# Kernel tuning notes

Measured on AMD Instinct MI355X. Metric: run time of the kernel, lower is better.

## Reference

```python
import jax, jax.numpy as jnp
import numpy as np

B = 100000  # number of index rows
R1, N1, N2, N3, R2 = 1, 200, 200, 50, 32


def setup_inputs() -> dict:
    key = jax.random.key(0)
    k0, k1, k2, k3, k4 = jax.random.split(key, 5)
    TT_core = jax.random.normal(k0, (R1, N1, N2, N3, R2), dtype=jnp.float32)
    # Kernel (gram) matrices per mode, as produced by e.g. an RBF kernel on
    # side information; positive entries in [0,1) like an RBF gram matrix.
    K1 = jax.random.uniform(k1, (N1, N1), dtype=jnp.float32)
    K2 = jax.random.uniform(k2, (N2, N2), dtype=jnp.float32)
    K3 = jax.random.uniform(k3, (N3, N3), dtype=jnp.float32)
    # Multi-index: one column per tensor mode; kept in [0, 50) so it is
    # in-range for every mode (N3 = 50 is the smallest).
    indices = jax.random.randint(k4, (B, 3), 0, N3, dtype=jnp.int64)
    return {"TT_core": TT_core, "K1": K1, "K2": K2, "K3": K3, "indices": indices}


def reference(TT_core, K1, K2, K3, indices):
    # lazy_mode_product(T, K, mode) == contract K over the given tensor mode.
    # TT_core axes: (r1, i, j, k, r2)
    T = jnp.einsum('ai,rijks->rajks', K1, TT_core)   # mode 1
    T = jnp.einsum('bj,rajks->rabks', K2, T)         # mode 2
    T = jnp.einsum('ck,rabks->rabcs', K3, T)         # mode 3
    # Auxiliary regularization term (full_grad=False branch of TT_kernel_component)
    reg = T * TT_core
    # T.permute([1,2,3,0,-1])[i1,i2,i3] -> (B, r1, r2) multi-index gather
    Tp = jnp.transpose(T, (1, 2, 3, 0, 4))           # (n1, n2, n3, r1, r2)
    out = Tp[indices[:, 0], indices[:, 1], indices[:, 2]]  # (B, r1, r2)
    return out, reg
```

## Files before the change

### kernel.cpp

```cpp
#include <hip/hip_runtime.h>
#include <type_traits>


typedef float    f32x4 __attribute__((ext_vector_type(4)));
typedef float    f32x8 __attribute__((ext_vector_type(8)));
typedef _Float16 half8 __attribute__((ext_vector_type(8)));
typedef unsigned short ushort8 __attribute__((ext_vector_type(8)));
typedef unsigned short u16;
typedef unsigned int   u32;

#define N12   200
#define N3    50
#define R2    32
#define SJK   320000
#define SKS   1600
#define NTOT  64000000
#define OUT_ELEMS 3200000
#define APAD  208
#define KPAD  224
#define K3B_HALVES 4096

__global__ __launch_bounds__(256) void k_prep(
    const float* __restrict__ K1, const float* __restrict__ K2,
    const float* __restrict__ K3, u16* __restrict__ kh) {
  int t = blockIdx.x * 256 + threadIdx.x;
  const int total = APAD * KPAD;
  if (t >= 2 * total + K3B_HALVES) return;
  float x;
  if (t < 2 * total) {
    const float* src = (t < total) ? K1 : K2;
    int tt = (t < total) ? t : t - total;
    int r = tt / KPAD, c = tt % KPAD;
    x = (r < N12 && c < N12) ? src[r * N12 + c] : 0.f;
  } else {
    int u = t - 2 * total;
    int e = u & 7, l = (u >> 3) & 63, frag = u >> 9;
    int c = (frag & 3) * 16 + (l & 15);
    int k = (frag >> 2) * 32 + (l >> 4) * 8 + e;
    x = (c < N3 && k < N3) ? K3[c * N3 + k] : 0.f;
  }
  kh[t] = __builtin_bit_cast(u16, (_Float16)x);
}

#define ALOAD(S)                                                              \
  { ar0 = *(const int4*)(Ah + ((wave*4+0)*16 + arow) * KPAD + (S)*32 + acolh); \
    ar1 = *(const int4*)(Ah + ((wave*4+1)*16 + arow) * KPAD + (S)*32 + acolh); \
    ar2 = *(const int4*)(Ah + ((wave*4+2)*16 + arow) * KPAD + (S)*32 + acolh); \
    ar3 = *(const int4*)(Ah + ((wave*4+3)*16 + arow) * KPAD + (S)*32 + acolh); }

#define ASTORE(BUF)                                                           \
  { *(int4*)(&As[BUF][(wave*4+0)*512 + lane*8]) = ar0;                        \
    *(int4*)(&As[BUF][(wave*4+1)*512 + lane*8]) = ar1;                        \
    *(int4*)(&As[BUF][(wave*4+2)*512 + lane*8]) = ar2;                        \
    *(int4*)(&As[BUF][(wave*4+3)*512 + lane*8]) = ar3; }

#define LOADB(S, BV)                                                          \
  { _Pragma("unroll")                                                         \
    for (int e = 0; e < 8; ++e) {                                             \
      int kr = (S)*32 + kq + e; if (kr > 199) kr = 199;                       \
      BV[e] = bp[(long)kr * ldB]; } }

#define STAGE(S, BV)                                                          \
  { half8 bh;                                                                 \
    _Pragma("unroll")                                                         \
    for (int e = 0; e < 8; ++e) {                                             \
      if constexpr (BF32) bh[e] = (_Float16)BV[e];                            \
      else bh[e] = __builtin_bit_cast(_Float16, (u16)BV[e]);                  \
    }                                                                         \
    const u16* as_ = &As[(S)&1][0];                                           \
    _Pragma("unroll")                                                         \
    for (int t = 0; t < 13; ++t) {                                            \
      half8 ah = *(const half8*)(as_ + (t*16 + l15)*32 + kq);                 \
      acc[t] = __builtin_amdgcn_mfma_f32_16x16x32_f16(ah, bh, acc[t], 0,0,0); \
    } }

template <typename BT, typename DT>
__global__ __launch_bounds__(256, 3) void k_mfma_contract(
    const BT* __restrict__ Bsrc, const u16* __restrict__ Ah,
    DT* __restrict__ Dout, int ldB, int ldD, long bStrideB, long bStrideD) {
  constexpr bool BF32 = std::is_same_v<BT, float>;
  __shared__ __align__(16) u16 As[2][8192];
  const int lane = threadIdx.x & 63;
  const int wave = threadIdx.x >> 6;
  const int l15  = lane & 15;
  const int kg   = lane >> 4;
  const int kq   = kg * 8;
  const int arow = lane >> 2;
  const int acolh = (lane & 3) * 8;
  const int n0   = blockIdx.x * 64 + wave * 16 + l15;
  const long bb  = (long)blockIdx.y * bStrideB;
  const long db  = (long)blockIdx.y * bStrideD;
  const BT* bp = Bsrc + bb + n0;

  f32x4 acc[13];
#pragma unroll
  for (int t = 0; t < 13; ++t)
#pragma unroll
    for (int q = 0; q < 4; ++q) acc[t][q] = 0.f;

  int4 ar0, ar1, ar2, ar3;
  using BReg = std::conditional_t<BF32, f32x8, ushort8>;
  BReg B0, B1, B2, B3, B4, B5, B6;

  ALOAD(0)
  LOADB(0, B0) LOADB(1, B1) LOADB(2, B2) LOADB(3, B3)
  LOADB(4, B4) LOADB(5, B5) LOADB(6, B6)
  ASTORE(0)
  __syncthreads();

  ALOAD(1)  STAGE(0, B0)  ASTORE(1)  __syncthreads();
  ALOAD(2)  STAGE(1, B1)  ASTORE(0)  __syncthreads();
  ALOAD(3)  STAGE(2, B2)  ASTORE(1)  __syncthreads();
  ALOAD(4)  STAGE(3, B3)  ASTORE(0)  __syncthreads();
  ALOAD(5)  STAGE(4, B4)  ASTORE(1)  __syncthreads();
  ALOAD(6)  STAGE(5, B5)  ASTORE(0)  __syncthreads();
  STAGE(6, B6)

#pragma unroll
  for (int t = 0; t < 13; ++t) {
    const int rb = t * 16 + kg * 4;
#pragma unroll
    for (int r = 0; r < 4; ++r) {
      const int row = rb + r;
      if (row < N12) {
        if constexpr (std::is_same_v<DT, float>)
          Dout[db + (long)row * ldD + n0] = acc[t][r];
        else
          Dout[db + (long)row * ldD + n0] =
              __builtin_bit_cast(u16, (_Float16)acc[t][r]);
      }
    }
  }
}

__global__ __launch_bounds__(256, 8) void k_contract_k_mfma(
    const u16* __restrict__ T2h, const float* __restrict__ TT,
    const u16* __restrict__ K3B, float* __restrict__ reg) {
  __shared__ __align__(16) u16 bs[K3B_HALVES];
  const int tid  = threadIdx.x;
  {
    const int4* src = (const int4*)K3B;
    int4* dst = (int4*)bs;
    dst[tid] = src[tid];
    dst[tid + 256] = src[tid + 256];
  }
  const int lane = tid & 63;
  const int wave = tid >> 6;
  const int l15  = lane & 15;
  const int kg   = lane >> 4;
  const int ab   = blockIdx.x * 4 + wave;
  const int base = ab * SKS;
  __syncthreads();

  half8 bf[2][4];
#pragma unroll
  for (int ks = 0; ks < 2; ++ks)
#pragma unroll
    for (int cs = 0; cs < 4; ++cs)
      bf[ks][cs] = *(const half8*)(bs + ((ks * 4 + cs) * 64 + lane) * 8);

  half8 af[2][2];
#pragma unroll
  for (int rt = 0; rt < 2; ++rt)
#pragma unroll
    for (int ks = 0; ks < 2; ++ks)
#pragma unroll
      for (int e = 0; e < 8; ++e) {
        int k = ks * 32 + kg * 8 + e; if (k > 49) k = 49;
        af[rt][ks][e] =
            __builtin_bit_cast(_Float16, T2h[base + k * R2 + rt * 16 + l15]);
      }

  f32x4 acc[2][4];
#pragma unroll
  for (int rt = 0; rt < 2; ++rt)
#pragma unroll
    for (int cs = 0; cs < 4; ++cs)
#pragma unroll
      for (int q = 0; q < 4; ++q) acc[rt][cs][q] = 0.f;

#pragma unroll
  for (int rt = 0; rt < 2; ++rt)
#pragma unroll
    for (int ks = 0; ks < 2; ++ks)
#pragma unroll
      for (int cs = 0; cs < 4; ++cs)
        acc[rt][cs] = __builtin_amdgcn_mfma_f32_16x16x32_f16(
            af[rt][ks], bf[ks][cs], acc[rt][cs], 0, 0, 0);

#pragma unroll
  for (int cs = 0; cs < 4; ++cs) {
    const int c = cs * 16 + l15;
    if (c < N3) {
      const int o0 = base + c * R2 + kg * 4;
      f32x4 tv0 = *(const f32x4*)(TT + o0);
      f32x4 tv1 = *(const f32x4*)(TT + o0 + 16);
      f32x4 r0, r1;
#pragma unroll
      for (int q = 0; q < 4; ++q) {
        r0[q] = acc[0][cs][q] * tv0[q];
        r1[q] = acc[1][cs][q] * tv1[q];
      }
      *(f32x4*)(reg + o0) = r0;
      *(f32x4*)(reg + o0 + 16) = r1;
    }
  }
}

template <typename T>
__global__ __launch_bounds__(256) void k_gather(
    const T* T2, const float* __restrict__ K3,
    const int* __restrict__ idx, float* __restrict__ out) {
  int g = blockIdx.x * 256 + threadIdx.x;
  int n = g >> 5, s = g & 31;
  int a = idx[n * 3 + 0], b = idx[n * 3 + 1], c = idx[n * 3 + 2];
  const T* t2 = T2 + a * SJK + b * SKS + s;
  const float* k3r = K3 + c * N3;
  float acc = 0.f;
#pragma unroll
  for (int k = 0; k < N3; ++k) {
    float v;
    if constexpr (std::is_same_v<T, float>) v = t2[k * R2];
    else v = (float)__builtin_bit_cast(_Float16, t2[k * R2]);
    acc = fmaf(k3r[k], v, acc);
  }
  out[g] = acc;
}

__global__ __launch_bounds__(256) void k_transpose(
    const float* __restrict__ K2, float* __restrict__ K2T) {
  int t = blockIdx.x * 256 + threadIdx.x;
  if (t < N12 * N12) {
    int i = t / N12, a = t % N12;
    K2T[t] = K2[a * N12 + i];
  }
}

__global__ __launch_bounds__(256) void k_contract_j_inplace(
    float* T12, const float* __restrict__ K2T) {
  __shared__ float lds[N12 * 80];
  const int a    = blockIdx.y;
  const int m0   = blockIdx.x * 80;
  const int base = a * SJK + m0;
  for (int t = threadIdx.x; t < N12 * 80; t += 256) {
    int j = t / 80, ml = t % 80;
    lds[t] = T12[base + j * SKS + ml];
  }
  __syncthreads();
  for (int o = threadIdx.x; o < N12 * 80; o += 256) {
    int b = o / 80, ml = o % 80;
    float acc = 0.f;
#pragma unroll 4
    for (int j = 0; j < N12; ++j)
      acc = fmaf(K2T[j * N12 + b], lds[j * 80 + ml], acc);
    T12[base + b * SKS + ml] = acc;
  }
}

__global__ __launch_bounds__(256) void k_contract_k_reg(
    const float* T2, const float* __restrict__ TT,
    const float* __restrict__ K3, float* reg) {
  const int t  = blockIdx.x * 256 + threadIdx.x;
  const int s  = t & 31;
  const int ab = t >> 5;
  const int base = ab * SKS + s;
  float v[N3];
#pragma unroll
  for (int k = 0; k < N3; ++k) v[k] = T2[base + k * R2];
  for (int c = 0; c < N3; ++c) {
    const float* k3r = K3 + c * N3;
    float a0 = 0.f, a1 = 0.f, a2 = 0.f, a3 = 0.f;
#pragma unroll
    for (int k = 0; k < 48; k += 4) {
      a0 = fmaf(k3r[k],     v[k],     a0);
      a1 = fmaf(k3r[k + 1], v[k + 1], a1);
      a2 = fmaf(k3r[k + 2], v[k + 2], a2);
      a3 = fmaf(k3r[k + 3], v[k + 3], a3);
    }
    a0 = fmaf(k3r[48], v[48], a0);
    a1 = fmaf(k3r[49], v[49], a1);
    const int o = base + c * R2;
    reg[o] = ((a0 + a1) + (a2 + a3)) * TT[o];
  }
}

extern "C" void kernel_launch(void* const* d_in, const int* in_sizes, int n_in,
                              void* d_out, int out_size, void* d_ws, size_t ws_size,
                              hipStream_t stream) {
  const float* TT  = (const float*)d_in[0];
  const float* K1  = (const float*)d_in[1];
  const float* K2  = (const float*)d_in[2];
  const float* K3  = (const float*)d_in[3];
  const int*   idx = (const int*)d_in[4];

  float* out = (float*)d_out;
  float* reg = out + OUT_ELEMS;
  u16* kh = (u16*)d_out;
  const int matoff = APAD * KPAD;
  const u16* k3b = kh + 2 * matoff;

  k_prep<<<dim3((2 * matoff + K3B_HALVES + 255) / 256), 256, 0, stream>>>(
      K1, K2, K3, kh);

  const size_t need = (size_t)NTOT * sizeof(u16);
  if (ws_size >= need) {
    u16* T1h = (u16*)reg;
    u16* T2h = (u16*)d_ws;
    k_mfma_contract<float, u16><<<dim3(SJK / 64, 1), 256, 0, stream>>>(
        TT, kh, T1h, SJK, SJK, 0L, 0L);
    k_mfma_contract<u16, u16><<<dim3(SKS / 64, N12), 256, 0, stream>>>(
        T1h, kh + matoff, T2h, SKS, SKS, (long)SJK, (long)SJK);
    k_contract_k_mfma<<<dim3(40000 / 4), 256, 0, stream>>>(T2h, TT, k3b, reg);
    k_gather<u16><<<dim3(OUT_ELEMS / 256), 256, 0, stream>>>(T2h, K3, idx, out);
  } else {
    float* k2t = out + 2 * OUT_ELEMS / 32;
    k_mfma_contract<float, float><<<dim3(SJK / 64, 1), 256, 0, stream>>>(
        TT, kh, reg, SJK, SJK, 0L, 0L);
    k_transpose<<<dim3((N12 * N12 + 255) / 256), 256, 0, stream>>>(K2, k2t);
    k_contract_j_inplace<<<dim3(20, N12), 256, 0, stream>>>(reg, k2t);
    k_gather<float><<<dim3(OUT_ELEMS / 256), 256, 0, stream>>>(reg, K3, idx, out);
    k_contract_k_reg<<<dim3(40000 * 32 / 256), 256, 0, stream>>>(reg, TT, K3, reg);
  }
}
```

Measured before the change: 403.0 us.

## Stage A operand in two large swizzled LDS chunks instead of per-slice double buffer

Replaces the seven-step double-buffered A slice pipeline, which had one barrier per 32-wide K slice, with two bulk loads of the fp16 A matrix into a larger LDS tile (128 K columns, then the remaining 96). The LDS layout uses an XOR-like rotation of 8-element chunks by row to avoid bank conflicts on the MFMA fragment reads. This cuts the barriers to three and removes the per-slice register staging. In exchange it uses more shared memory per block, about 53KB against 32KB before, which may lower occupancy, and the A loads are no longer overlapped with the MFMA work.

```diff
diff --git a/kernel.cpp b/kernel.cpp
--- a/kernel.cpp
+++ b/kernel.cpp
@@ -42,35 +42,22 @@
   kh[t] = __builtin_bit_cast(u16, (_Float16)x);
 }
 
-#define ALOAD(S)                                                              \
-  { ar0 = *(const int4*)(Ah + ((wave*4+0)*16 + arow) * KPAD + (S)*32 + acolh); \
-    ar1 = *(const int4*)(Ah + ((wave*4+1)*16 + arow) * KPAD + (S)*32 + acolh); \
-    ar2 = *(const int4*)(Ah + ((wave*4+2)*16 + arow) * KPAD + (S)*32 + acolh); \
-    ar3 = *(const int4*)(Ah + ((wave*4+3)*16 + arow) * KPAD + (S)*32 + acolh); }
-
-#define ASTORE(BUF)                                                           \
-  { *(int4*)(&As[BUF][(wave*4+0)*512 + lane*8]) = ar0;                        \
-    *(int4*)(&As[BUF][(wave*4+1)*512 + lane*8]) = ar1;                        \
-    *(int4*)(&As[BUF][(wave*4+2)*512 + lane*8]) = ar2;                        \
-    *(int4*)(&As[BUF][(wave*4+3)*512 + lane*8]) = ar3; }
-
 #define LOADB(S, BV)                                                          \
   { _Pragma("unroll")                                                         \
     for (int e = 0; e < 8; ++e) {                                             \
       int kr = (S)*32 + kq + e; if (kr > 199) kr = 199;                       \
       BV[e] = bp[(long)kr * ldB]; } }
 
-#define STAGE(S, BV)                                                          \
+#define STAGE(SL, BV)                                                         \
   { half8 bh;                                                                 \
     _Pragma("unroll")                                                         \
     for (int e = 0; e < 8; ++e) {                                             \
       if constexpr (BF32) bh[e] = (_Float16)BV[e];                            \
       else bh[e] = __builtin_bit_cast(_Float16, (u16)BV[e]);                  \
     }                                                                         \
-    const u16* as_ = &As[(S)&1][0];                                           \
     _Pragma("unroll")                                                         \
     for (int t = 0; t < 13; ++t) {                                            \
-      half8 ah = *(const half8*)(as_ + (t*16 + l15)*32 + kq);                 \
+      half8 ah = *(const half8*)(As + (t*16 + l15)*128 + (SL)*32 + rdc);      \
       acc[t] = __builtin_amdgcn_mfma_f32_16x16x32_f16(ah, bh, acc[t], 0,0,0); \
     } }
 
@@ -79,14 +66,14 @@
     const BT* __restrict__ Bsrc, const u16* __restrict__ Ah,
     DT* __restrict__ Dout, int ldB, int ldD, long bStrideB, long bStrideD) {
   constexpr bool BF32 = std::is_same_v<BT, float>;
-  __shared__ __align__(16) u16 As[2][8192];
-  const int lane = threadIdx.x & 63;
-  const int wave = threadIdx.x >> 6;
+  __shared__ __align__(16) u16 As[APAD * 128];
+  const int tid  = threadIdx.x;
+  const int lane = tid & 63;
+  const int wave = tid >> 6;
   const int l15  = lane & 15;
   const int kg   = lane >> 4;
   const int kq   = kg * 8;
-  const int arow = lane >> 2;
-  const int acolh = (lane & 3) * 8;
+  const int rdc  = ((kg + (l15 >> 1)) & 3) * 8;
   const int n0   = blockIdx.x * 64 + wave * 16 + l15;
   const long bb  = (long)blockIdx.y * bStrideB;
   const long db  = (long)blockIdx.y * bStrideD;
@@ -98,23 +85,33 @@
 #pragma unroll
     for (int q = 0; q < 4; ++q) acc[t][q] = 0.f;
 
-  int4 ar0, ar1, ar2, ar3;
   using BReg = std::conditional_t<BF32, f32x8, ushort8>;
   BReg B0, B1, B2, B3, B4, B5, B6;
 
-  ALOAD(0)
+#pragma unroll
+  for (int it = 0; it < 13; ++it) {
+    int u = tid + it * 256;
+    int row = u >> 4, c16 = u & 15;
+    int sl = c16 >> 2, c4 = c16 & 3;
+    int4 v = *(const int4*)(Ah + row * KPAD + c16 * 8);
+    *(int4*)(&As[row * 128 + sl * 32 + ((c4 + (row >> 1)) & 3) * 8]) = v;
+  }
   LOADB(0, B0) LOADB(1, B1) LOADB(2, B2) LOADB(3, B3)
   LOADB(4, B4) LOADB(5, B5) LOADB(6, B6)
-  ASTORE(0)
-  __syncthreads();
-
-  ALOAD(1)  STAGE(0, B0)  ASTORE(1)  __syncthreads();
-  ALOAD(2)  STAGE(1, B1)  ASTORE(0)  __syncthreads();
-  ALOAD(3)  STAGE(2, B2)  ASTORE(1)  __syncthreads();
-  ALOAD(4)  STAGE(3, B3)  ASTORE(0)  __syncthreads();
-  ALOAD(5)  STAGE(4, B4)  ASTORE(1)  __syncthreads();
-  ALOAD(6)  STAGE(5, B5)  ASTORE(0)  __syncthreads();
-  STAGE(6, B6)
+  __syncthreads();
+
+  STAGE(0, B0)  STAGE(1, B1)  STAGE(2, B2)  STAGE(3, B3)
+  __syncthreads();
+
+  for (int u = tid; u < APAD * 12; u += 256) {
+    int row = u / 12, c12 = u - row * 12;
+    int sl = c12 >> 2, c4 = c12 & 3;
+    int4 v = *(const int4*)(Ah + row * KPAD + 128 + c12 * 8);
+    *(int4*)(&As[row * 128 + sl * 32 + ((c4 + (row >> 1)) & 3) * 8]) = v;
+  }
+  __syncthreads();
+
+  STAGE(0, B4)  STAGE(1, B5)  STAGE(2, B6)
 
 #pragma unroll
   for (int t = 0; t < 13; ++t) {
```

Result: slower. 443.8 us (+10.1%).
